# Kernel tuning notes

Hardware: AMD Instinct MI355X
Metric: run time of the kernel (lower is better)

The kernel has to match this reference:

```python
import jax, jax.numpy as jnp
import numpy as np

N, IN_DIM, HID, NCLS = 100000, 512, 128, 10
ALPHA = 0.2  # LeakyReLU negative slope

def _xavier_normal(key, shape, gain=1.414):
    fan_in, fan_out = shape[0], shape[1]
    std = gain * (2.0 / (fan_in + fan_out)) ** 0.5
    return (jax.random.normal(key, shape, jnp.float32) * std).astype(jnp.float32)

def setup_inputs() -> dict:
    key = jax.random.key(0)
    k1, k2, k3, k4, k5, k6 = jax.random.split(key, 6)
    features = jax.random.normal(k1, (N, IN_DIM), jnp.float32)
    # learned params per init_kwargs (xavier_normal with gain=1.414 as in torch)
    C = _xavier_normal(k2, (IN_DIM, HID))
    W = _xavier_normal(k3, (2 * HID, HID))
    V = _xavier_normal(k4, (HID, NCLS))
    # per-node top-2 neighbors from sortNodes(weight_dict[idx]); the buggy
    # `while len(...) < 2` loop never runs, so only the first merge matters.
    n1_idx = jax.random.randint(k5, (N,), 0, N, dtype=jnp.int64 if jax.config.read('jax_enable_x64') else jnp.int32)
    n2_idx = jax.random.randint(k6, (N,), 0, N, dtype=n1_idx.dtype)
    return {"features": features, "C": C, "W": W, "V": V,
            "n1_idx": n1_idx, "n2_idx": n2_idx}

def reference(features, C, W, V, n1_idx, n2_idx):
    # h = features @ C : [N, H]
    h = features @ C
    # For every node, the effective output of the Huffman merge loop is the
    # single merge of its two top-sorted neighbors (duplicated if degree 1):
    # concat(h[n1], h[n2]) @ W. Split W into halves to avoid materializing [N, 2H].
    W1, W2 = W[:HID], W[HID:]                      # each [H, H]
    outs = h[n1_idx] @ W1 + h[n2_idx] @ W2         # [N, H]
    results = jax.nn.leaky_relu(outs @ V, negative_slope=ALPHA)  # [N, num_class]
    return jax.nn.log_softmax(results, axis=1)
```

## Files before the change

kernel.cpp:

```cpp
#include <hip/hip_runtime.h>
#include <hip/hip_bf16.h>
#include <stdint.h>

#define NROWS 100000
#define INDIM 512
#define HID 128
#define NCLS 10
#define LEAKY_ALPHA 0.2f

typedef __bf16 bf16x8_t __attribute__((ext_vector_type(8)));
typedef __bf16 bf16x4_t __attribute__((ext_vector_type(4)));
typedef float f32x4_t __attribute__((ext_vector_type(4)));
typedef unsigned short ushort8_t __attribute__((ext_vector_type(8)));

union Frag {
    bf16x8_t v8;
    bf16x4_t v4[2];
    unsigned short u[8];
};

__device__ __forceinline__ unsigned short f2bf(float x) {
    union { __hip_bfloat16 b; unsigned short u; } cv;
    cv.b = __float2bfloat16(x);
    return cv.u;
}

__device__ __forceinline__ float bf2f(unsigned short u) {
    union { float f; unsigned int i; } v;
    v.i = ((unsigned int)u) << 16;
    return v.f;
}

__device__ __forceinline__ int img_addr(int r, int kk) {
    int p = r >> 1;
    int o = ((r & 1) << 6) | (kk << 1);
    return (p << 7) | ((((o >> 4) ^ (p & 7)) << 4) | (o & 15));
}

__device__ __forceinline__ void gload_lds16(const void* g, void* l) {
    __builtin_amdgcn_global_load_lds(
        (const __attribute__((address_space(1))) unsigned int*)g,
        (__attribute__((address_space(3))) unsigned int*)l, 16, 0, 0);
}

__global__ __launch_bounds__(256) void k_prep(
    const float* __restrict__ C, const float* __restrict__ W, const float* __restrict__ V,
    unsigned short* __restrict__ Qimg) {
    __shared__ float Vl[HID * NCLS];
    __shared__ float Pl[2][HID][10];
    __shared__ float Cl[32][132];

    const int tid = threadIdx.x, b = blockIdx.x;
    for (int i = tid; i < HID * NCLS; i += 256) Vl[i] = V[i];
    __syncthreads();

    {
        const int half = tid >> 7, j = tid & 127;
        const float* wr = W + (half * HID + j) * HID;
        float s[NCLS];
#pragma unroll
        for (int c = 0; c < NCLS; ++c) s[c] = 0.f;
        for (int m = 0; m < HID; m += 4) {
            float4 wv = *reinterpret_cast<const float4*>(wr + m);
            float wa[4] = {wv.x, wv.y, wv.z, wv.w};
#pragma unroll
            for (int u = 0; u < 4; ++u)
#pragma unroll
                for (int c = 0; c < NCLS; ++c) s[c] += wa[u] * Vl[(m + u) * NCLS + c];
        }
#pragma unroll
        for (int c = 0; c < NCLS; ++c) Pl[half][j][c] = s[c];
    }
    const int k0 = b << 5;
    {
        const int kr = tid >> 3, ns = (tid & 7) << 4;
        const float4* src = reinterpret_cast<const float4*>(C + (k0 + kr) * HID + ns);
#pragma unroll
        for (int j = 0; j < 4; ++j)
            *reinterpret_cast<float4*>(&Cl[kr][ns + 4 * j]) = src[j];
    }
    __syncthreads();

    for (int e = tid; e < 32 * 32; e += 256) {
        const int n = e >> 5, kl = e & 31;
        const int half = n >> 4, c = n & 15;
        float s = 0.f;
        if (c < NCLS) {
#pragma unroll 4
            for (int j = 0; j < HID; ++j) s += Cl[kl][j] * Pl[half][j][c];
        }
        *(unsigned short*)((char*)Qimg + b * 2048 + img_addr(n, kl)) = f2bf(s);
    }
}

__global__ __launch_bounds__(256, 4) void k_gemm(
    const float* __restrict__ A,
    const unsigned short* __restrict__ Qimg,
    unsigned short* __restrict__ G)
{
    __shared__ unsigned short Qs[16384];
    __shared__ unsigned short As[4096];

    const int tid  = threadIdx.x;
    const int w    = tid >> 6;
    const int lane = tid & 63;
    const int l15  = lane & 15;
    const int kg   = (lane >> 4) << 2;
    const long row0 = (long)blockIdx.x * 128;
    const int phase = blockIdx.x & 15;

#pragma unroll
    for (int j = 0; j < 8; ++j) {
        const int off = (j * 4 + w) * 1024;
        gload_lds16((const char*)Qimg + off + lane * 16, (char*)Qs + off);
    }

    const int ar_s = tid >> 1;
    const int kh   = (tid & 1) << 4;
    long gr = row0 + ar_s;
    if (gr >= NROWS) gr = NROWS - 1;
    const float* asrc = A + gr * INDIM + kh;
    const int aw0 = img_addr(ar_s, kh);
    const int aw1 = img_addr(ar_s, kh + 8);

    int ard0[2], ard1[2], brd0[2], brd1[2];
#pragma unroll
    for (int ii = 0; ii < 2; ++ii) {
        int r = w * 32 + ii * 16 + l15;
        ard0[ii] = img_addr(r, kg);
        ard1[ii] = img_addr(r, kg + 16);
    }
#pragma unroll
    for (int f = 0; f < 2; ++f) {
        brd0[f] = img_addr(f * 16 + l15, kg);
        brd1[f] = img_addr(f * 16 + l15, kg + 16);
    }

    f32x4_t acc[2][2];
#pragma unroll
    for (int i = 0; i < 2; ++i)
#pragma unroll
        for (int f = 0; f < 2; ++f)
#pragma unroll
            for (int r = 0; r < 4; ++r) acc[i][f][r] = 0.f;

    const char* asb = (const char*)&As[0];
    const char* bsb = (const char*)&Qs[0];

    float4 qA[4], qB[4];

    {
        const float* s0 = asrc + ((0 + phase) & 15) * 32;
        float4 v[4];
#pragma unroll
        for (int j = 0; j < 4; ++j) v[j] = *reinterpret_cast<const float4*>(s0 + 4 * j);
        ushort8_t lo, hi;
#pragma unroll
        for (int e = 0; e < 4; ++e) {
            lo[e] = f2bf(v[0][e]); lo[4 + e] = f2bf(v[1][e]);
            hi[e] = f2bf(v[2][e]); hi[4 + e] = f2bf(v[3][e]);
        }
        *(ushort8_t*)((char*)asb + aw0) = lo;
        *(ushort8_t*)((char*)asb + aw1) = hi;
    }
    {
        const float* s1 = asrc + ((1 + phase) & 15) * 32;
#pragma unroll
        for (int j = 0; j < 4; ++j) qB[j] = *reinterpret_cast<const float4*>(s1 + 4 * j);
        const float* s2 = asrc + ((2 + phase) & 15) * 32;
#pragma unroll
        for (int j = 0; j < 4; ++j) qA[j] = *reinterpret_cast<const float4*>(s2 + 4 * j);
    }
    __syncthreads();

#pragma unroll
    for (int t = 0; t < 16; ++t) {
        const int pt = (t + phase) & 15;

        Frag fa[2], fb[2];
#pragma unroll
        for (int ii = 0; ii < 2; ++ii) {
            fa[ii].v4[0] = *(const bf16x4_t*)(asb + ard0[ii]);
            fa[ii].v4[1] = *(const bf16x4_t*)(asb + ard1[ii]);
        }
#pragma unroll
        for (int f = 0; f < 2; ++f) {
            fb[f].v4[0] = *(const bf16x4_t*)(bsb + pt * 2048 + brd0[f]);
            fb[f].v4[1] = *(const bf16x4_t*)(bsb + pt * 2048 + brd1[f]);
        }
#pragma unroll
        for (int ii = 0; ii < 2; ++ii)
#pragma unroll
            for (int f = 0; f < 2; ++f)
                acc[ii][f] = __builtin_amdgcn_mfma_f32_16x16x32_bf16(fa[ii].v8, fb[f].v8, acc[ii][f], 0, 0, 0);

        if (t < 15) {
            const int slot = (t + 1) & 1;
            ushort8_t lo, hi;
            if (slot == 1) {
#pragma unroll
                for (int e = 0; e < 4; ++e) {
                    lo[e] = f2bf(qB[0][e]); lo[4 + e] = f2bf(qB[1][e]);
                    hi[e] = f2bf(qB[2][e]); hi[4 + e] = f2bf(qB[3][e]);
                }
            } else {
#pragma unroll
                for (int e = 0; e < 4; ++e) {
                    lo[e] = f2bf(qA[0][e]); lo[4 + e] = f2bf(qA[1][e]);
                    hi[e] = f2bf(qA[2][e]); hi[4 + e] = f2bf(qA[3][e]);
                }
            }
            *(ushort8_t*)((char*)asb + aw0) = lo;
            *(ushort8_t*)((char*)asb + aw1) = hi;

            if (t + 3 <= 15) {
                const float* src = asrc + (((t + 3) + phase) & 15) * 32;
                if (slot == 1) {
#pragma unroll
                    for (int j = 0; j < 4; ++j) qB[j] = *reinterpret_cast<const float4*>(src + 4 * j);
                } else {
#pragma unroll
                    for (int j = 0; j < 4; ++j) qA[j] = *reinterpret_cast<const float4*>(src + 4 * j);
                }
            }
        }
    }

    const int rq_ = (lane >> 4) << 2;
#pragma unroll
    for (int ii = 0; ii < 2; ++ii)
#pragma unroll
        for (int r = 0; r < 4; ++r) {
            long grow = row0 + w * 32 + ii * 16 + rq_ + r;
            if (l15 < NCLS && grow < NROWS) {
                G[grow * 32 + l15]      = f2bf(acc[ii][0][r]);
                G[grow * 32 + 16 + l15] = f2bf(acc[ii][1][r]);
            }
        }
}

__global__ __launch_bounds__(256) void k_epi(
    const unsigned short* __restrict__ G,
    const int* __restrict__ n1, const int* __restrict__ n2,
    float* __restrict__ Out) {
    const long i = (long)blockIdx.x * 256 + threadIdx.x;
    if (i >= NROWS) return;
    const ushort8_t* p1 = (const ushort8_t*)(G + (long)n1[i] * 32);
    const ushort8_t* p2 = (const ushort8_t*)(G + (long)n2[i] * 32 + 16);
    ushort8_t a0 = p1[0], a1 = p1[1];
    ushort8_t b0 = p2[0], b1 = p2[1];

    float x[NCLS];
#pragma unroll
    for (int c = 0; c < 8; ++c) x[c] = bf2f(a0[c]) + bf2f(b0[c]);
    x[8] = bf2f(a1[0]) + bf2f(b1[0]);
    x[9] = bf2f(a1[1]) + bf2f(b1[1]);

    float m = -1e30f;
#pragma unroll
    for (int c = 0; c < NCLS; ++c) {
        x[c] = (x[c] >= 0.f) ? x[c] : LEAKY_ALPHA * x[c];
        m = fmaxf(m, x[c]);
    }
    float sum = 0.f;
#pragma unroll
    for (int c = 0; c < NCLS; ++c) sum += __expf(x[c] - m);
    const float lse = m + __logf(sum);
    float2* o = (float2*)(Out + i * NCLS);
#pragma unroll
    for (int j = 0; j < 5; ++j) {
        float2 v = {x[2 * j] - lse, x[2 * j + 1] - lse};
        o[j] = v;
    }
}

extern "C" void kernel_launch(void* const* d_in, const int* in_sizes, int n_in,
                              void* d_out, int out_size, void* d_ws, size_t ws_size,
                              hipStream_t stream) {
    const float* features = (const float*)d_in[0];
    const float* C  = (const float*)d_in[1];
    const float* W  = (const float*)d_in[2];
    const float* V  = (const float*)d_in[3];
    const int*   n1 = (const int*)d_in[4];
    const int*   n2 = (const int*)d_in[5];
    float* out = (float*)d_out;

    char* ws = (char*)d_ws;
    unsigned short* Qimg = (unsigned short*)ws;
    unsigned short* G = (unsigned short*)(ws + 32768);

    hipLaunchKernelGGL(k_prep, dim3(16), dim3(256), 0, stream, C, W, V, Qimg);
    hipLaunchKernelGGL(k_gemm, dim3((NROWS + 127) / 128), dim3(256), 0, stream,
                       features, Qimg, G);
    hipLaunchKernelGGL(k_epi, dim3((NROWS + 255) / 256), dim3(256), 0, stream,
                       G, n1, n2, out);
}
```

Before: 67.08 us.

## Deepen A-tile prefetch to four stages, recoalesce loads, spread prep over more blocks

```diff
diff --git a/kernel.cpp b/kernel.cpp
--- a/kernel.cpp
+++ b/kernel.cpp
@@ -11,6 +11,7 @@
 typedef __bf16 bf16x8_t __attribute__((ext_vector_type(8)));
 typedef __bf16 bf16x4_t __attribute__((ext_vector_type(4)));
 typedef float f32x4_t __attribute__((ext_vector_type(4)));
+typedef unsigned short ushort4_t __attribute__((ext_vector_type(4)));
 typedef unsigned short ushort8_t __attribute__((ext_vector_type(8)));
 
 union Frag {
@@ -48,7 +49,7 @@
     unsigned short* __restrict__ Qimg) {
     __shared__ float Vl[HID * NCLS];
     __shared__ float Pl[2][HID][10];
-    __shared__ float Cl[32][132];
+    __shared__ float Cl[8][132];
 
     const int tid = threadIdx.x, b = blockIdx.x;
     for (int i = tid; i < HID * NCLS; i += 256) Vl[i] = V[i];
@@ -71,25 +72,24 @@
 #pragma unroll
         for (int c = 0; c < NCLS; ++c) Pl[half][j][c] = s[c];
     }
-    const int k0 = b << 5;
-    {
-        const int kr = tid >> 3, ns = (tid & 7) << 4;
-        const float4* src = reinterpret_cast<const float4*>(C + (k0 + kr) * HID + ns);
-#pragma unroll
-        for (int j = 0; j < 4; ++j)
-            *reinterpret_cast<float4*>(&Cl[kr][ns + 4 * j]) = src[j];
+    const int k0 = b << 3;
+    {
+        const int kr = tid >> 5, ns = (tid & 31) << 2;
+        *reinterpret_cast<float4*>(&Cl[kr][ns]) =
+            *reinterpret_cast<const float4*>(C + (k0 + kr) * HID + ns);
     }
     __syncthreads();
 
-    for (int e = tid; e < 32 * 32; e += 256) {
-        const int n = e >> 5, kl = e & 31;
+    {
+        const int n = tid >> 3, kl = tid & 7;
         const int half = n >> 4, c = n & 15;
         float s = 0.f;
         if (c < NCLS) {
 #pragma unroll 4
             for (int j = 0; j < HID; ++j) s += Cl[kl][j] * Pl[half][j][c];
         }
-        *(unsigned short*)((char*)Qimg + b * 2048 + img_addr(n, kl)) = f2bf(s);
+        const int k = k0 + kl, t = k >> 5, kk = k & 31;
+        *(unsigned short*)((char*)Qimg + t * 2048 + img_addr(n, kk)) = f2bf(s);
     }
 }
 
@@ -107,7 +107,6 @@
     const int l15  = lane & 15;
     const int kg   = (lane >> 4) << 2;
     const long row0 = (long)blockIdx.x * 128;
-    const int phase = blockIdx.x & 15;
 
 #pragma unroll
     for (int j = 0; j < 8; ++j) {
@@ -115,13 +114,17 @@
         gload_lds16((const char*)Qimg + off + lane * 16, (char*)Qs + off);
     }
 
-    const int ar_s = tid >> 1;
-    const int kh   = (tid & 1) << 4;
-    long gr = row0 + ar_s;
-    if (gr >= NROWS) gr = NROWS - 1;
-    const float* asrc = A + gr * INDIM + kh;
-    const int aw0 = img_addr(ar_s, kh);
-    const int aw1 = img_addr(ar_s, kh + 8);
+    const int kseg = (lane & 7) << 2;
+    const float* asrc_[4];
+    int awr_[4];
+#pragma unroll
+    for (int j = 0; j < 4; ++j) {
+        const int lr = w * 32 + j * 8 + (lane >> 3);
+        long gr = row0 + lr;
+        if (gr >= NROWS) gr = NROWS - 1;
+        asrc_[j] = A + gr * INDIM + kseg;
+        awr_[j] = img_addr(lr, kseg);
+    }
 
     int ard0[2], ard1[2], brd0[2], brd1[2];
 #pragma unroll
@@ -147,36 +150,38 @@
     const char* asb = (const char*)&As[0];
     const char* bsb = (const char*)&Qs[0];
 
-    float4 qA[4], qB[4];
-
-    {
-        const float* s0 = asrc + ((0 + phase) & 15) * 32;
+    float4 qA[4], qB[4], qC[4], qD[4];
+
+#define CVT_STORE(q)                                                         \
+    {                                                                        \
+        _Pragma("unroll")                                                    \
+        for (int j = 0; j < 4; ++j) {                                        \
+            ushort4_t pk;                                                    \
+            _Pragma("unroll")                                                \
+            for (int e = 0; e < 4; ++e) pk[e] = f2bf(q[j][e]);               \
+            *(ushort4_t*)((char*)asb + awr_[j]) = pk;                        \
+        }                                                                    \
+    }
+#define LOADQ(q, off)                                                        \
+    {                                                                        \
+        _Pragma("unroll")                                                    \
+        for (int j = 0; j < 4; ++j)                                          \
+            q[j] = *reinterpret_cast<const float4*>(asrc_[j] + (off));       \
+    }
+
+    {
         float4 v[4];
-#pragma unroll
-        for (int j = 0; j < 4; ++j) v[j] = *reinterpret_cast<const float4*>(s0 + 4 * j);
-        ushort8_t lo, hi;
-#pragma unroll
-        for (int e = 0; e < 4; ++e) {
-            lo[e] = f2bf(v[0][e]); lo[4 + e] = f2bf(v[1][e]);
-            hi[e] = f2bf(v[2][e]); hi[4 + e] = f2bf(v[3][e]);
-        }
-        *(ushort8_t*)((char*)asb + aw0) = lo;
-        *(ushort8_t*)((char*)asb + aw1) = hi;
-    }
-    {
-        const float* s1 = asrc + ((1 + phase) & 15) * 32;
-#pragma unroll
-        for (int j = 0; j < 4; ++j) qB[j] = *reinterpret_cast<const float4*>(s1 + 4 * j);
-        const float* s2 = asrc + ((2 + phase) & 15) * 32;
-#pragma unroll
-        for (int j = 0; j < 4; ++j) qA[j] = *reinterpret_cast<const float4*>(s2 + 4 * j);
-    }
+        LOADQ(v, 0)
+        CVT_STORE(v)
+    }
+    LOADQ(qB, 32)
+    LOADQ(qC, 64)
+    LOADQ(qD, 96)
+    LOADQ(qA, 128)
     __syncthreads();
 
 #pragma unroll
     for (int t = 0; t < 16; ++t) {
-        const int pt = (t + phase) & 15;
-
         Frag fa[2], fb[2];
 #pragma unroll
         for (int ii = 0; ii < 2; ++ii) {
@@ -185,8 +190,8 @@
         }
 #pragma unroll
         for (int f = 0; f < 2; ++f) {
-            fb[f].v4[0] = *(const bf16x4_t*)(bsb + pt * 2048 + brd0[f]);
-            fb[f].v4[1] = *(const bf16x4_t*)(bsb + pt * 2048 + brd1[f]);
+            fb[f].v4[0] = *(const bf16x4_t*)(bsb + t * 2048 + brd0[f]);
+            fb[f].v4[1] = *(const bf16x4_t*)(bsb + t * 2048 + brd1[f]);
         }
 #pragma unroll
         for (int ii = 0; ii < 2; ++ii)
@@ -195,33 +200,18 @@
                 acc[ii][f] = __builtin_amdgcn_mfma_f32_16x16x32_bf16(fa[ii].v8, fb[f].v8, acc[ii][f], 0, 0, 0);
 
         if (t < 15) {
-            const int slot = (t + 1) & 1;
-            ushort8_t lo, hi;
-            if (slot == 1) {
-#pragma unroll
-                for (int e = 0; e < 4; ++e) {
-                    lo[e] = f2bf(qB[0][e]); lo[4 + e] = f2bf(qB[1][e]);
-                    hi[e] = f2bf(qB[2][e]); hi[4 + e] = f2bf(qB[3][e]);
-                }
-            } else {
-#pragma unroll
-                for (int e = 0; e < 4; ++e) {
-                    lo[e] = f2bf(qA[0][e]); lo[4 + e] = f2bf(qA[1][e]);
-                    hi[e] = f2bf(qA[2][e]); hi[4 + e] = f2bf(qA[3][e]);
-                }
-            }
-            *(ushort8_t*)((char*)asb + aw0) = lo;
-            *(ushort8_t*)((char*)asb + aw1) = hi;
-
-            if (t + 3 <= 15) {
-                const float* src = asrc + (((t + 3) + phase) & 15) * 32;
-                if (slot == 1) {
-#pragma unroll
-                    for (int j = 0; j < 4; ++j) qB[j] = *reinterpret_cast<const float4*>(src + 4 * j);
-                } else {
-#pragma unroll
-                    for (int j = 0; j < 4; ++j) qA[j] = *reinterpret_cast<const float4*>(src + 4 * j);
-                }
+            const int slot = (t + 1) & 3;
+            if (slot == 0)      { CVT_STORE(qA) }
+            else if (slot == 1) { CVT_STORE(qB) }
+            else if (slot == 2) { CVT_STORE(qC) }
+            else                { CVT_STORE(qD) }
+
+            if (t + 5 <= 15) {
+                const int off = (t + 5) * 32;
+                if (slot == 0)      { LOADQ(qA, off) }
+                else if (slot == 1) { LOADQ(qB, off) }
+                else if (slot == 2) { LOADQ(qC, off) }
+                else                { LOADQ(qD, off) }
             }
         }
     }
@@ -289,7 +279,7 @@
     unsigned short* Qimg = (unsigned short*)ws;
     unsigned short* G = (unsigned short*)(ws + 32768);
 
-    hipLaunchKernelGGL(k_prep, dim3(16), dim3(256), 0, stream, C, W, V, Qimg);
+    hipLaunchKernelGGL(k_prep, dim3(64), dim3(256), 0, stream, C, W, V, Qimg);
     hipLaunchKernelGGL(k_gemm, dim3((NROWS + 127) / 128), dim3(256), 0, stream,
                        features, Qimg, G);
     hipLaunchKernelGGL(k_epi, dim3((NROWS + 255) / 256), dim3(256), 0, stream,
```

Result: faster. 56.34 us (-16.0%).
